# Optimization experiments

Hardware: AMD Instinct MI355X
Metric: run time of the kernel (lower is better)

The kernel has to match this reference:

```python
import jax, jax.numpy as jnp
import numpy as np

N = 8192
IN_F = 256
OUT_F = 64
ALPHA = 0.3  # LeakyReLU negative slope
NEG_INF = -9e15


def setup_inputs() -> dict:
    key = jax.random.key(0)
    k1, k2, k3, k4 = jax.random.split(key, 4)
    h = jax.random.normal(k1, (N, IN_F), dtype=jnp.float32)
    # sparse-ish binary adjacency with self loops (values are 0/1 floats)
    adj = (jax.random.uniform(k2, (N, N)) < 0.05).astype(jnp.float32)
    adj = jnp.maximum(adj, jnp.eye(N, dtype=jnp.float32))
    # xavier_uniform-style scales (gain=1.414)
    w_lim = 1.414 * np.sqrt(6.0 / (IN_F + OUT_F))
    a_lim = 1.414 * np.sqrt(6.0 / (2 * OUT_F + 1))
    W = jax.random.uniform(k3, (IN_F, OUT_F), minval=-w_lim, maxval=w_lim, dtype=jnp.float32)
    a = jax.random.uniform(k4, (2 * OUT_F, 1), minval=-a_lim, maxval=a_lim, dtype=jnp.float32)
    return {"h": h, "adj": adj, "W": W, "a": a}


def reference(h, adj, W, a):
    # Wh: [N, F]
    Wh = h @ W
    # Additive decomposition of the original concat-attention:
    # e_ij = leakyrelu(a[:F].Wh_i + a[F:].Wh_j)  -- identical math, no NxNx2F tensor
    src = Wh @ a[:OUT_F]      # [N, 1]
    dst = Wh @ a[OUT_F:]      # [N, 1]
    e = jax.nn.leaky_relu(src + dst.T, negative_slope=ALPHA)  # [N, N]
    e = e * adj               # faithful: original multiplies by adj before masking
    att = jnp.where(adj > 0, e, NEG_INF)
    att = jax.nn.softmax(att, axis=1)
    # dropout omitted (eval mode / deterministic reference)
    h_prime = att @ Wh        # [N, F]
    return jax.nn.elu(h_prime)
```

## Files before the change

### kernel.cpp

```cpp
#include <hip/hip_runtime.h>
#include <hip/hip_bf16.h>

#define N_NODES 8192
#define IN_F    256
#define OUT_F   64
#define ALPHA   0.3f
#define MBIAS   20.0f
#define CSPL    8
#define COLS_PER (N_NODES / CSPL)
#define NTILES  (COLS_PER / 64)
#define MST     17
#define WH_BLOCKS (N_NODES / 16)

typedef unsigned short u16;
typedef unsigned int   u32;
typedef unsigned long long u64;
typedef __attribute__((ext_vector_type(8))) short bf16x8;
typedef __attribute__((ext_vector_type(4))) float f32x4;

__device__ __forceinline__ float bf2f(u32 u) { return __uint_as_float(u << 16); }
__device__ __forceinline__ u32 f2bfbits(float x) {
    u32 u = __float_as_uint(x);
    return (u + 0x7FFFu + ((u >> 16) & 1u)) >> 16;
}
__device__ __forceinline__ float lrelu(float s) { return s > 0.f ? s : ALPHA * s; }

__device__ __forceinline__ int detect_bf16(const void* adj) {
    return ((((const u32*)adj)[0] & 0xFFFFu) == 0x3F80u) ? 1 : 0;
}

template <bool BF16>
__device__ __forceinline__ float ld(const void* p, size_t idx) {
    if constexpr (BF16) return bf2f(((const u16*)p)[idx]);
    else                return ((const float*)p)[idx];
}

template <bool BF16>
__device__ __forceinline__ void wh4_impl(
    const void* __restrict__ h, const void* __restrict__ W,
    const void* __restrict__ a, float* __restrict__ src,
    float* __restrict__ dst, int i0, int lane, float* accv)
{
    float acc0 = 0.f, acc1 = 0.f, acc2 = 0.f, acc3 = 0.f;
#pragma unroll 8
    for (int k = 0; k < IN_F; ++k) {
        float wv = ld<BF16>(W, (size_t)k * OUT_F + lane);
        float h0 = ld<BF16>(h, (size_t)(i0 + 0) * IN_F + k);
        float h1 = ld<BF16>(h, (size_t)(i0 + 1) * IN_F + k);
        float h2 = ld<BF16>(h, (size_t)(i0 + 2) * IN_F + k);
        float h3 = ld<BF16>(h, (size_t)(i0 + 3) * IN_F + k);
        acc0 = fmaf(h0, wv, acc0);
        acc1 = fmaf(h1, wv, acc1);
        acc2 = fmaf(h2, wv, acc2);
        acc3 = fmaf(h3, wv, acc3);
    }
    float av = ld<BF16>(a, lane);
    float bv = ld<BF16>(a, OUT_F + lane);
    float accs[4] = {acc0, acc1, acc2, acc3};
#pragma unroll
    for (int r = 0; r < 4; ++r) {
        float ps = accs[r] * av, pd = accs[r] * bv;
#pragma unroll
        for (int off = 32; off > 0; off >>= 1) {
            ps += __shfl_xor(ps, off, 64);
            pd += __shfl_xor(pd, off, 64);
        }
        if (lane == 0) { src[i0 + r] = ps; dst[i0 + r] = pd; }
        accv[r] = accs[r];
    }
}

__global__ __launch_bounds__(256) void gat_prep_kernel(
    const void* __restrict__ h, const void* __restrict__ W,
    const void* __restrict__ a, const void* __restrict__ adj,
    u16* __restrict__ WhB, float* __restrict__ src, float* __restrict__ dst,
    u64* __restrict__ mask64)
{
    __shared__ float accs[16][OUT_F];
    const int tid = threadIdx.x, wave = tid >> 6, lane = tid & 63;
    const int isbf = detect_bf16(adj);

    if (blockIdx.x < WH_BLOCKS) {
        const int i0 = blockIdx.x * 16 + wave * 4;
        float av[4];
        if (isbf) wh4_impl<true >(h, W, a, src, dst, i0, lane, av);
        else      wh4_impl<false>(h, W, a, src, dst, i0, lane, av);
#pragma unroll
        for (int r = 0; r < 4; ++r) accs[wave * 4 + r][lane] = av[r];
        __syncthreads();

        const int T = blockIdx.x >> 2, q = blockIdx.x & 3;
        const int nt = wave, n = lane & 15, kg = lane >> 4;
        if ((kg >> 1) == (q & 1)) {
            const int ln0 = (kg & 1) * 8;
            u32 w[4];
#pragma unroll
            for (int e = 0; e < 4; ++e) {
                u32 lo = f2bfbits(accs[ln0 + 2 * e][nt * 16 + n]);
                u32 hi = f2bfbits(accs[ln0 + 2 * e + 1][nt * 16 + n]);
                w[e] = lo | (hi << 16);
            }
            u16* out = WhB + ((size_t)T * 8 + nt * 2 + (q >> 1)) * 512 + lane * 8;
            *(uint4*)out = *(uint4*)w;
        }
    } else {
        const int wgid = (blockIdx.x - WH_BLOCKS) * 4 + wave;
        const int NW   = 2048 * 4;
        const int C    = (N_NODES / 256) * N_NODES;
        if (isbf) {
            const u16* base = (const u16*)adj;
            for (int c = wgid; c < C; c += NW) {
                const u16* p = base + (size_t)c * 256;
                u64 b0 = __ballot(p[lane]       != 0);
                u64 b1 = __ballot(p[64  + lane] != 0);
                u64 b2 = __ballot(p[128 + lane] != 0);
                u64 b3 = __ballot(p[192 + lane] != 0);
                u64 v = (lane == 0) ? b0 : (lane == 1) ? b1 : (lane == 2) ? b2 : b3;
                if (lane < 4) mask64[(size_t)c * 4 + lane] = v;
            }
        } else {
            const float* base = (const float*)adj;
            for (int c = wgid; c < C; c += NW) {
                const float* p = base + (size_t)c * 256;
                u64 b0 = __ballot(p[lane]       != 0.f);
                u64 b1 = __ballot(p[64  + lane] != 0.f);
                u64 b2 = __ballot(p[128 + lane] != 0.f);
                u64 b3 = __ballot(p[192 + lane] != 0.f);
                u64 v = (lane == 0) ? b0 : (lane == 1) ? b1 : (lane == 2) ? b2 : b3;
                if (lane < 4) mask64[(size_t)c * 4 + lane] = v;
            }
        }
    }
}

__global__ __launch_bounds__(256, 4) void gat_attn_kernel(
    const u64* __restrict__ mask64, const u16* __restrict__ WhB,
    const float* __restrict__ src, const float* __restrict__ dst,
    float* __restrict__ O_part, float* __restrict__ l_part)
{
    __shared__ alignas(16) u64  Mlds[64 * MST];
    __shared__ alignas(16) float Dlds[COLS_PER];

    const int tid = threadIdx.x, wave = tid >> 6, lane = tid & 63;
    const int i0 = blockIdx.x * 64, c0 = blockIdx.y * COLS_PER;

    {
        const int r = tid >> 2, q = tid & 3;
        const u64* g = mask64 + (size_t)(i0 + r) * (N_NODES / 64) + (c0 >> 6) + q * 4;
        *(uint4*)&Mlds[r * MST + q * 4]     = *(const uint4*)g;
        *(uint4*)&Mlds[r * MST + q * 4 + 2] = *(const uint4*)(g + 2);
    }
#pragma unroll
    for (int q = 0; q < COLS_PER / 256; ++q)
        Dlds[q * 256 + tid] = dst[c0 + q * 256 + tid];

    __syncthreads();

    const int mrow = lane & 15, kq = (lane >> 4) * 8;
    const int mloc = 16 * wave + mrow;
    const float srow = src[i0 + mloc];
    const float mbound = lrelu(srow + MBIAS);

    const u16* fb = WhB + (size_t)(blockIdx.y * NTILES) * 4096 + lane * 8;

    f32x4 acc[4] = {{0,0,0,0},{0,0,0,0},{0,0,0,0},{0,0,0,0}};
    f32x4 acc_l  = {0, 0, 0, 0};
    union { u32 w[4]; bf16x8 v; } ones;
    ones.w[0] = 0x3F803F80u; ones.w[1] = 0x3F803F80u;
    ones.w[2] = 0x3F803F80u; ones.w[3] = 0x3F803F80u;

    uint4 bc0 = *(const uint4*)(fb);
    uint4 bc1 = *(const uint4*)(fb + 1024);
    uint4 bc2 = *(const uint4*)(fb + 2048);
    uint4 bc3 = *(const uint4*)(fb + 3072);

    for (int s = 0; s < 2 * NTILES; ++s) {
        const int t = s >> 1, ks = s & 1;

        uint4 bn0, bn1, bn2, bn3;
        if (s + 1 < 2 * NTILES) {
            const int off = ((s + 1) >> 1) * 4096 + ((s + 1) & 1) * 512;
            bn0 = *(const uint4*)(fb + off);
            bn1 = *(const uint4*)(fb + off + 1024);
            bn2 = *(const uint4*)(fb + off + 2048);
            bn3 = *(const uint4*)(fb + off + 3072);
        }

        const u64 mword = Mlds[mloc * MST + t];
        const u32 bits = (u32)(mword >> (ks * 32 + kq)) & 0xFFu;
        const float* dp = &Dlds[t * 64 + ks * 32 + kq];
        float4 dd0 = *(const float4*)dp;
        float4 dd1 = *(const float4*)(dp + 4);
        float dv[8] = {dd0.x,dd0.y,dd0.z,dd0.w, dd1.x,dd1.y,dd1.z,dd1.w};
        union { u32 w[4]; bf16x8 v; } pa;
#pragma unroll
        for (int e = 0; e < 4; ++e) {
            float s0 = srow + dv[2 * e];
            float s1 = srow + dv[2 * e + 1];
            s0 = fmaxf(s0, ALPHA * s0) - mbound;
            s1 = fmaxf(s1, ALPHA * s1) - mbound;
            float p0 = __expf(s0);
            float p1 = __expf(s1);
            p0 = (bits & (1u << (2 * e)))     ? p0 : 0.f;
            p1 = (bits & (1u << (2 * e + 1))) ? p1 : 0.f;
            u32 pw;
            asm("v_cvt_pk_bf16_f32 %0, %1, %2" : "=v"(pw) : "v"(p0), "v"(p1));
            pa.w[e] = pw;
        }

        acc_l  = __builtin_amdgcn_mfma_f32_16x16x32_bf16(pa.v, ones.v, acc_l, 0, 0, 0);

        acc[0] = __builtin_amdgcn_mfma_f32_16x16x32_bf16(pa.v, *(bf16x8*)&bc0, acc[0], 0, 0, 0);
        acc[1] = __builtin_amdgcn_mfma_f32_16x16x32_bf16(pa.v, *(bf16x8*)&bc1, acc[1], 0, 0, 0);
        acc[2] = __builtin_amdgcn_mfma_f32_16x16x32_bf16(pa.v, *(bf16x8*)&bc2, acc[2], 0, 0, 0);
        acc[3] = __builtin_amdgcn_mfma_f32_16x16x32_bf16(pa.v, *(bf16x8*)&bc3, acc[3], 0, 0, 0);

        bc0 = bn0; bc1 = bn1; bc2 = bn2; bc3 = bn3;
    }

    if ((lane & 15) == 0) {
        float* lp = l_part + (size_t)blockIdx.y * N_NODES + i0 + 16 * wave + (lane >> 4) * 4;
#pragma unroll
        for (int reg = 0; reg < 4; ++reg) lp[reg] = acc_l[reg];
    }

    float* Ob = O_part + (size_t)blockIdx.y * N_NODES * OUT_F;
#pragma unroll
    for (int nt = 0; nt < 4; ++nt)
#pragma unroll
        for (int reg = 0; reg < 4; ++reg) {
            int row = i0 + 16 * wave + (lane >> 4) * 4 + reg;
            int col = 16 * nt + (lane & 15);
            Ob[(size_t)row * OUT_F + col] = acc[nt][reg];
        }
}

__global__ __launch_bounds__(256) void gat_reduce_kernel(
    const float* __restrict__ O_part, const float* __restrict__ l_part,
    const void* __restrict__ adj, void* __restrict__ out)
{
    int gid = blockIdx.x * 256 + threadIdx.x;
    int i = gid >> 6;
    float O = 0.f, L = 0.f;
#pragma unroll
    for (int c = 0; c < CSPL; ++c) {
        O += O_part[(size_t)c * N_NODES * OUT_F + gid];
        L += l_part[c * N_NODES + i];
    }
    float hp = O / L;
    float o = hp > 0.f ? hp : expm1f(hp);
    if (detect_bf16(adj)) ((u16*)out)[gid] = (u16)f2bfbits(o);
    else                  ((float*)out)[gid] = o;
}

extern "C" void kernel_launch(void* const* d_in, const int* in_sizes, int n_in,
                              void* d_out, int out_size, void* d_ws, size_t ws_size,
                              hipStream_t stream)
{
    const void* h   = d_in[0];
    const void* adj = d_in[1];
    const void* W   = d_in[2];
    const void* a   = d_in[3];

    char* ws = (char*)d_ws;
    u16*   WhB    = (u16*)ws;
    float* src    = (float*)(ws + (1u << 20));
    float* dst    = (float*)(ws + (1u << 20) + 32768);
    u64*   mask64 = (u64*)  (ws + (3u << 20));
    float* O_part = (float*)(ws + (16u << 20));
    float* l_part = (float*)(ws + (32u << 20));

    gat_prep_kernel<<<WH_BLOCKS + 2048, 256, 0, stream>>>(h, W, a, adj, WhB, src, dst, mask64);
    dim3 grid(N_NODES / 64, CSPL);
    gat_attn_kernel<<<grid, 256, 0, stream>>>(mask64, WhB, src, dst, O_part, l_part);
    gat_reduce_kernel<<<N_NODES * OUT_F / 256, 256, 0, stream>>>(O_part, l_part, adj, d_out);
}
```

Measured before the change: 415.3 us.

## Fuse adjacency bitmask construction into attention kernel, drop mask64 buffer

Adjacency-to-bitmask compression moves out of the prep kernel and into the attention kernel, which now reads its 64x1024 adj tile directly and ballots it into LDS. This removes the global mask64 write and read-back and shrinks the prep grid. In exchange, each attention block issues strided adj loads before compute, which lengthens its prologue and may expose load latency that was previously spread across a separate memory-bound pass.

```diff
diff --git a/kernel.cpp b/kernel.cpp
--- a/kernel.cpp
+++ b/kernel.cpp
@@ -73,82 +73,77 @@
 __global__ __launch_bounds__(256) void gat_prep_kernel(
     const void* __restrict__ h, const void* __restrict__ W,
     const void* __restrict__ a, const void* __restrict__ adj,
-    u16* __restrict__ WhB, float* __restrict__ src, float* __restrict__ dst,
-    u64* __restrict__ mask64)
+    u16* __restrict__ WhB, float* __restrict__ src, float* __restrict__ dst)
 {
     __shared__ float accs[16][OUT_F];
     const int tid = threadIdx.x, wave = tid >> 6, lane = tid & 63;
     const int isbf = detect_bf16(adj);
 
-    if (blockIdx.x < WH_BLOCKS) {
-        const int i0 = blockIdx.x * 16 + wave * 4;
-        float av[4];
-        if (isbf) wh4_impl<true >(h, W, a, src, dst, i0, lane, av);
-        else      wh4_impl<false>(h, W, a, src, dst, i0, lane, av);
-#pragma unroll
-        for (int r = 0; r < 4; ++r) accs[wave * 4 + r][lane] = av[r];
-        __syncthreads();
-
-        const int T = blockIdx.x >> 2, q = blockIdx.x & 3;
-        const int nt = wave, n = lane & 15, kg = lane >> 4;
-        if ((kg >> 1) == (q & 1)) {
-            const int ln0 = (kg & 1) * 8;
-            u32 w[4];
-#pragma unroll
-            for (int e = 0; e < 4; ++e) {
-                u32 lo = f2bfbits(accs[ln0 + 2 * e][nt * 16 + n]);
-                u32 hi = f2bfbits(accs[ln0 + 2 * e + 1][nt * 16 + n]);
-                w[e] = lo | (hi << 16);
-            }
-            u16* out = WhB + ((size_t)T * 8 + nt * 2 + (q >> 1)) * 512 + lane * 8;
-            *(uint4*)out = *(uint4*)w;
-        }
-    } else {
-        const int wgid = (blockIdx.x - WH_BLOCKS) * 4 + wave;
-        const int NW   = 2048 * 4;
-        const int C    = (N_NODES / 256) * N_NODES;
+    const int i0 = blockIdx.x * 16 + wave * 4;
+    float av[4];
+    if (isbf) wh4_impl<true >(h, W, a, src, dst, i0, lane, av);
+    else      wh4_impl<false>(h, W, a, src, dst, i0, lane, av);
+#pragma unroll
+    for (int r = 0; r < 4; ++r) accs[wave * 4 + r][lane] = av[r];
+    __syncthreads();
+
+    const int T = blockIdx.x >> 2, q = blockIdx.x & 3;
+    const int nt = wave, n = lane & 15, kg = lane >> 4;
+    if ((kg >> 1) == (q & 1)) {
+        const int ln0 = (kg & 1) * 8;
+        u32 w[4];
+#pragma unroll
+        for (int e = 0; e < 4; ++e) {
+            u32 lo = f2bfbits(accs[ln0 + 2 * e][nt * 16 + n]);
+            u32 hi = f2bfbits(accs[ln0 + 2 * e + 1][nt * 16 + n]);
+            w[e] = lo | (hi << 16);
+        }
+        u16* out = WhB + ((size_t)T * 8 + nt * 2 + (q >> 1)) * 512 + lane * 8;
+        *(uint4*)out = *(uint4*)w;
+    }
+}
+
+__global__ __launch_bounds__(256, 4) void gat_attn_kernel(
+    const void* __restrict__ adj, const u16* __restrict__ WhB,
+    const float* __restrict__ src, const float* __restrict__ dst,
+    float* __restrict__ O_part, float* __restrict__ l_part)
+{
+    __shared__ alignas(16) u64  Mlds[64 * MST];
+    __shared__ alignas(16) float Dlds[COLS_PER];
+
+    const int tid = threadIdx.x, wave = tid >> 6, lane = tid & 63;
+    const int i0 = blockIdx.x * 64, c0 = blockIdx.y * COLS_PER;
+    const int isbf = detect_bf16(adj);
+
+    {
+        const int rbase = wave * 16;
         if (isbf) {
-            const u16* base = (const u16*)adj;
-            for (int c = wgid; c < C; c += NW) {
-                const u16* p = base + (size_t)c * 256;
+            const u16* ab = (const u16*)adj;
+#pragma unroll 2
+            for (int it = 0; it < 64; ++it) {
+                const int r = rbase + (it >> 2), ch = it & 3;
+                const u16* p = ab + (size_t)(i0 + r) * N_NODES + c0 + ch * 256;
                 u64 b0 = __ballot(p[lane]       != 0);
                 u64 b1 = __ballot(p[64  + lane] != 0);
                 u64 b2 = __ballot(p[128 + lane] != 0);
                 u64 b3 = __ballot(p[192 + lane] != 0);
                 u64 v = (lane == 0) ? b0 : (lane == 1) ? b1 : (lane == 2) ? b2 : b3;
-                if (lane < 4) mask64[(size_t)c * 4 + lane] = v;
+                if (lane < 4) Mlds[r * MST + ch * 4 + lane] = v;
             }
         } else {
-            const float* base = (const float*)adj;
-            for (int c = wgid; c < C; c += NW) {
-                const float* p = base + (size_t)c * 256;
+            const float* ab = (const float*)adj;
+#pragma unroll 2
+            for (int it = 0; it < 64; ++it) {
+                const int r = rbase + (it >> 2), ch = it & 3;
+                const float* p = ab + (size_t)(i0 + r) * N_NODES + c0 + ch * 256;
                 u64 b0 = __ballot(p[lane]       != 0.f);
                 u64 b1 = __ballot(p[64  + lane] != 0.f);
                 u64 b2 = __ballot(p[128 + lane] != 0.f);
                 u64 b3 = __ballot(p[192 + lane] != 0.f);
                 u64 v = (lane == 0) ? b0 : (lane == 1) ? b1 : (lane == 2) ? b2 : b3;
-                if (lane < 4) mask64[(size_t)c * 4 + lane] = v;
+                if (lane < 4) Mlds[r * MST + ch * 4 + lane] = v;
             }
         }
-    }
-}
-
-__global__ __launch_bounds__(256, 4) void gat_attn_kernel(
-    const u64* __restrict__ mask64, const u16* __restrict__ WhB,
-    const float* __restrict__ src, const float* __restrict__ dst,
-    float* __restrict__ O_part, float* __restrict__ l_part)
-{
-    __shared__ alignas(16) u64  Mlds[64 * MST];
-    __shared__ alignas(16) float Dlds[COLS_PER];
-
-    const int tid = threadIdx.x, wave = tid >> 6, lane = tid & 63;
-    const int i0 = blockIdx.x * 64, c0 = blockIdx.y * COLS_PER;
-
-    {
-        const int r = tid >> 2, q = tid & 3;
-        const u64* g = mask64 + (size_t)(i0 + r) * (N_NODES / 64) + (c0 >> 6) + q * 4;
-        *(uint4*)&Mlds[r * MST + q * 4]     = *(const uint4*)g;
-        *(uint4*)&Mlds[r * MST + q * 4 + 2] = *(const uint4*)(g + 2);
     }
 #pragma unroll
     for (int q = 0; q < COLS_PER / 256; ++q)
@@ -266,12 +261,11 @@
     u16*   WhB    = (u16*)ws;
     float* src    = (float*)(ws + (1u << 20));
     float* dst    = (float*)(ws + (1u << 20) + 32768);
-    u64*   mask64 = (u64*)  (ws + (3u << 20));
     float* O_part = (float*)(ws + (16u << 20));
     float* l_part = (float*)(ws + (32u << 20));
 
-    gat_prep_kernel<<<WH_BLOCKS + 2048, 256, 0, stream>>>(h, W, a, adj, WhB, src, dst, mask64);
+    gat_prep_kernel<<<WH_BLOCKS, 256, 0, stream>>>(h, W, a, adj, WhB, src, dst);
     dim3 grid(N_NODES / 64, CSPL);
-    gat_attn_kernel<<<grid, 256, 0, stream>>>(mask64, WhB, src, dst, O_part, l_part);
+    gat_attn_kernel<<<grid, 256, 0, stream>>>(adj, WhB, src, dst, O_part, l_part);
     gat_reduce_kernel<<<N_NODES * OUT_F / 256, 256, 0, stream>>>(O_part, l_part, adj, d_out);
 }
```

Result: slower. 426.1 us (+2.6%).
